# Kernel tuning notes

Measured on AMD Instinct MI355X. Metric: run time of the kernel, lower is better.

Reference implementation:

```python
import jax, jax.numpy as jnp
import numpy as np

B, Q, KV = 4, 256, 1024
QS, KS, H, VS = 128, 128, 128, 256

def setup_inputs() -> dict:
    key = jax.random.key(0)
    ks = jax.random.split(key, 7)
    return {
        "queries": jax.random.normal(ks[0], (B, Q, QS), dtype=jnp.float32),
        "keys": jax.random.normal(ks[1], (B, KV, KS), dtype=jnp.float32),
        "values": jax.random.normal(ks[2], (B, KV, VS), dtype=jnp.float32),
        "valid_lens": jax.random.randint(ks[3], (B,), 0, KV, dtype=jnp.int64 if jax.config.read('jax_enable_x64') else jnp.int32),
        "Wq": jax.random.normal(ks[4], (QS, H), dtype=jnp.float32),
        "Wk": jax.random.normal(ks[5], (KS, H), dtype=jnp.float32),
        "wv": jax.random.normal(ks[6], (H,), dtype=jnp.float32),
    }

def reference(queries, keys, values, valid_lens, Wq, Wk, wv):
    # project: [B,Q,H], [B,KV,H]
    q = jnp.einsum('bqd,dh->bqh', queries, Wq)
    k = jnp.einsum('bkd,dh->bkh', keys, Wk)
    # additive scores: broadcast add -> tanh -> reduce with w_v  [B,Q,KV]
    feats = jnp.tanh(q[:, :, None, :] + k[:, None, :, :])  # [B,Q,KV,H]
    scores = jnp.einsum('bqkh,h->bqk', feats, wv)
    # masked softmax over KV with value -1e6 at masked slots
    mask = jnp.arange(scores.shape[-1])[None, None, :] < valid_lens[:, None, None]
    scores = jnp.where(mask, scores, -1e6)
    attn = jax.nn.softmax(scores, axis=-1)
    # weighted sum of values  [B,Q,VS]
    return jnp.einsum('bqk,bkv->bqv', attn, values)
```

## Files before the change

kernel.cpp:

```cpp
#include <hip/hip_runtime.h>

#define C2LOG2E 2.8853900817779268f
#define LOG2E   1.4426950408889634f

__device__ __forceinline__ float sig2(float x) {
    return __builtin_amdgcn_rcpf(__builtin_amdgcn_exp2f(x) + 1.0f);
}

__global__ __launch_bounds__(256) void proj_kernel(
    const float* __restrict__ q_in, const float* __restrict__ k_in,
    const float* __restrict__ Wq, const float* __restrict__ Wk,
    float* __restrict__ qc, float* __restrict__ kct)
{
    __shared__ __align__(16) float x_s[8][128];
    __shared__ float ps[2][8][128];
    int tid = threadIdx.x;
    int blk = blockIdx.x;
    bool is_q = (blk < 128);
    int r0 = (is_q ? blk : blk - 128) * 8;
    const float* X = (is_q ? q_in : k_in) + (size_t)r0 * 128;
    const float* W = is_q ? Wq : Wk;

    {
        float4 v = ((const float4*)X)[tid];
        *(float4*)&x_s[tid >> 5][(tid & 31) * 4] = v;
    }
    __syncthreads();

    int h    = tid & 127;
    int half = tid >> 7;
    int d0   = half * 64;
    float acc[8] = {0,0,0,0,0,0,0,0};
#pragma unroll 2
    for (int i4 = 0; i4 < 16; ++i4) {
        int d = d0 + 4*i4;
        float w0 = W[(d+0)*128 + h];
        float w1 = W[(d+1)*128 + h];
        float w2 = W[(d+2)*128 + h];
        float w3 = W[(d+3)*128 + h];
#pragma unroll
        for (int r = 0; r < 8; ++r) {
            float4 xv = *(const float4*)&x_s[r][d];
            acc[r] = fmaf(xv.x, w0, fmaf(xv.y, w1,
                     fmaf(xv.z, w2, fmaf(xv.w, w3, acc[r]))));
        }
    }
#pragma unroll
    for (int r = 0; r < 8; ++r) ps[half][r][h] = acc[r];
    __syncthreads();

    int rq = tid >> 7;
    float v0 = (ps[0][rq*4+0][h] + ps[1][rq*4+0][h]) * C2LOG2E;
    float v1 = (ps[0][rq*4+1][h] + ps[1][rq*4+1][h]) * C2LOG2E;
    float v2 = (ps[0][rq*4+2][h] + ps[1][rq*4+2][h]) * C2LOG2E;
    float v3 = (ps[0][rq*4+3][h] + ps[1][rq*4+3][h]) * C2LOG2E;

    if (is_q) {
        qc[(size_t)(r0 + rq*4 + 0)*128 + h] = v0;
        qc[(size_t)(r0 + rq*4 + 1)*128 + h] = v1;
        qc[(size_t)(r0 + rq*4 + 2)*128 + h] = v2;
        qc[(size_t)(r0 + rq*4 + 3)*128 + h] = v3;
    } else {
        int bb = r0 >> 10;
        int c  = (r0 & 1023) >> 6;
        int i0 = (r0 & 63) + rq*4;
        float* dst = kct + (((size_t)(bb*16 + c))*128 + h)*64 + i0;
        *(float4*)dst = make_float4(v0, v1, v2, v3);
    }
}

__global__ __launch_bounds__(1024, 4) void attn_kernel(
    const float* __restrict__ qc, const float* __restrict__ kct,
    const float* __restrict__ values, const int* __restrict__ valid_lens,
    const float* __restrict__ wv, float* __restrict__ out)
{
    __shared__ float4 e4_s[1024];
    __shared__ float4 po8[8][4][64];
    __shared__ float4 red_m[16], red_s[16];

    int tid  = threadIdx.x;
    int b    = blockIdx.y;
    int q0   = blockIdx.x * 4;
    int w    = tid >> 6;
    int lane = tid & 63;
    int kv   = tid;
    int vl   = valid_lens[b];

    const float4* q40 = (const float4*)(qc + (size_t)(b*256 + q0)*128);
    const float4* wv4 = (const float4*)wv;
    const float* p = kct + ((size_t)(b*16 + w))*8192 + lane;

    float a[4] = {0,0,0,0};
    if (w*64 < vl) {
        for (int hb = 0; hb < 32; ++hb) {
            float4 wvv = wv4[hb];
            float4 k = make_float4(p[0], p[64], p[128], p[192]);
            p += 256;
#pragma unroll
            for (int q = 0; q < 4; ++q) {
                float4 qv = q40[q*32 + hb];
                a[q] = fmaf(wvv.x, sig2(qv.x + k.x), a[q]);
                a[q] = fmaf(wvv.y, sig2(qv.y + k.y), a[q]);
                a[q] = fmaf(wvv.z, sig2(qv.z + k.z), a[q]);
                a[q] = fmaf(wvv.w, sig2(qv.w + k.w), a[q]);
            }
        }
    }

    bool valid = (kv < vl);
    float s[4], m[4];
#pragma unroll
    for (int q = 0; q < 4; ++q) {
        s[q] = valid ? -2.f*a[q] : -1e6f;
        m[q] = s[q];
    }
#pragma unroll
    for (int off = 32; off; off >>= 1)
#pragma unroll
        for (int q = 0; q < 4; ++q) m[q] = fmaxf(m[q], __shfl_xor(m[q], off));
    if (lane == 0) red_m[w] = make_float4(m[0], m[1], m[2], m[3]);
    __syncthreads();
    {
        float4 mm = red_m[0];
#pragma unroll
        for (int ww = 1; ww < 16; ++ww) {
            float4 t = red_m[ww];
            mm.x = fmaxf(mm.x, t.x); mm.y = fmaxf(mm.y, t.y);
            mm.z = fmaxf(mm.z, t.z); mm.w = fmaxf(mm.w, t.w);
        }
        m[0] = mm.x; m[1] = mm.y; m[2] = mm.z; m[3] = mm.w;
    }

    float e[4], l[4];
#pragma unroll
    for (int q = 0; q < 4; ++q) {
        e[q] = __builtin_amdgcn_exp2f((s[q] - m[q]) * LOG2E);
        l[q] = e[q];
    }
    e4_s[kv] = make_float4(e[0], e[1], e[2], e[3]);
#pragma unroll
    for (int off = 32; off; off >>= 1)
#pragma unroll
        for (int q = 0; q < 4; ++q) l[q] += __shfl_xor(l[q], off);
    if (lane == 0) red_s[w] = make_float4(l[0], l[1], l[2], l[3]);
    __syncthreads();
    float inv[4];
    {
        float4 ss = red_s[0];
#pragma unroll
        for (int ww = 1; ww < 16; ++ww) {
            float4 t = red_s[ww];
            ss.x += t.x; ss.y += t.y; ss.z += t.z; ss.w += t.w;
        }
        inv[0] = 1.0f/ss.x; inv[1] = 1.0f/ss.y; inv[2] = 1.0f/ss.z; inv[3] = 1.0f/ss.w;
    }

    int kv_end = (vl == 0) ? 1024 : vl;
    float4 ac[4] = {{0,0,0,0},{0,0,0,0},{0,0,0,0},{0,0,0,0}};
    const float4* V4 = (const float4*)values + (size_t)b*65536 + lane;
#pragma unroll 2
    for (int k2 = w; k2 < kv_end; k2 += 16) {
        float4 vv = V4[(size_t)k2*64];
        float4 ee = e4_s[k2];
        ac[0].x = fmaf(ee.x, vv.x, ac[0].x); ac[0].y = fmaf(ee.x, vv.y, ac[0].y);
        ac[0].z = fmaf(ee.x, vv.z, ac[0].z); ac[0].w = fmaf(ee.x, vv.w, ac[0].w);
        ac[1].x = fmaf(ee.y, vv.x, ac[1].x); ac[1].y = fmaf(ee.y, vv.y, ac[1].y);
        ac[1].z = fmaf(ee.y, vv.z, ac[1].z); ac[1].w = fmaf(ee.y, vv.w, ac[1].w);
        ac[2].x = fmaf(ee.z, vv.x, ac[2].x); ac[2].y = fmaf(ee.z, vv.y, ac[2].y);
        ac[2].z = fmaf(ee.z, vv.z, ac[2].z); ac[2].w = fmaf(ee.z, vv.w, ac[2].w);
        ac[3].x = fmaf(ee.w, vv.x, ac[3].x); ac[3].y = fmaf(ee.w, vv.y, ac[3].y);
        ac[3].z = fmaf(ee.w, vv.z, ac[3].z); ac[3].w = fmaf(ee.w, vv.w, ac[3].w);
    }

    if (w >= 8) {
#pragma unroll
        for (int q = 0; q < 4; ++q) po8[w-8][q][lane] = ac[q];
    }
    __syncthreads();
    if (w < 8) {
#pragma unroll
        for (int q = 0; q < 4; ++q) {
            float4 t = po8[w][q][lane];
            t.x += ac[q].x; t.y += ac[q].y; t.z += ac[q].z; t.w += ac[q].w;
            po8[w][q][lane] = t;
        }
    }
    __syncthreads();

    int qq  = tid >> 8;
    int col = tid & 255;
    const float* pp = (const float*)po8;
    float r = 0.f;
#pragma unroll
    for (int ww = 0; ww < 8; ++ww) r += pp[(ww*4 + qq)*256 + col];
    out[((size_t)(b*256 + q0 + qq))*256 + col] = r * inv[qq];
}

extern "C" void kernel_launch(void* const* d_in, const int* in_sizes, int n_in,
                              void* d_out, int out_size, void* d_ws, size_t ws_size,
                              hipStream_t stream)
{
    const float* queries = (const float*)d_in[0];
    const float* keys    = (const float*)d_in[1];
    const float* values  = (const float*)d_in[2];
    const int*   vlens   = (const int*)d_in[3];
    const float* Wq      = (const float*)d_in[4];
    const float* Wk      = (const float*)d_in[5];
    const float* wv      = (const float*)d_in[6];
    float* out = (float*)d_out;

    float* qc  = (float*)d_ws;
    float* kct = qc + 4*256*128;

    proj_kernel<<<640, 256, 0, stream>>>(queries, keys, Wq, Wk, qc, kct);
    attn_kernel<<<dim3(64, 4), 1024, 0, stream>>>(qc, kct, values, vlens, wv, out);
}
```

Before: 106.3 us.

## Remap score phase to 2 queries x 2 KV chunks per wave with float4 key layout

```diff
diff --git a/kernel.cpp b/kernel.cpp
--- a/kernel.cpp
+++ b/kernel.cpp
@@ -64,8 +64,11 @@
         int bb = r0 >> 10;
         int c  = (r0 & 1023) >> 6;
         int i0 = (r0 & 63) + rq*4;
-        float* dst = kct + (((size_t)(bb*16 + c))*128 + h)*64 + i0;
-        *(float4*)dst = make_float4(v0, v1, v2, v3);
+        float* dst = kct + ((((size_t)(bb*16 + c))*32 + (h >> 2))*64 + i0)*4 + (h & 3);
+        dst[0]  = v0;
+        dst[4]  = v1;
+        dst[8]  = v2;
+        dst[12] = v3;
     }
 }
 
@@ -74,86 +77,108 @@
     const float* __restrict__ values, const int* __restrict__ valid_lens,
     const float* __restrict__ wv, float* __restrict__ out)
 {
-    __shared__ float4 e4_s[1024];
+    __shared__ float2 e2_s[2][1024];
     __shared__ float4 po8[8][4][64];
-    __shared__ float4 red_m[16], red_s[16];
+    __shared__ float2 red_m[16], red_s[16];
 
     int tid  = threadIdx.x;
     int b    = blockIdx.y;
     int q0   = blockIdx.x * 4;
     int w    = tid >> 6;
     int lane = tid & 63;
-    int kv   = tid;
+    int qh   = w >> 3;
+    int c0   = w & 7;
     int vl   = valid_lens[b];
 
-    const float4* q40 = (const float4*)(qc + (size_t)(b*256 + q0)*128);
+    const float4* qa4 = (const float4*)(qc + (size_t)(b*256 + q0 + 2*qh)*128);
+    const float4* qb4 = qa4 + 32;
     const float4* wv4 = (const float4*)wv;
-    const float* p = kct + ((size_t)(b*16 + w))*8192 + lane;
-
-    float a[4] = {0,0,0,0};
-    if (w*64 < vl) {
+    const float4* kb  = (const float4*)kct;
+    const float4* p0  = kb + ((size_t)(b*16 + c0))*2048 + lane;
+    const float4* p1  = p0 + 8*2048;
+
+    bool act0 = (c0*64 < vl);
+    bool act1 = ((c0 + 8)*64 < vl);
+    float a00=0.f, a10=0.f, a01=0.f, a11=0.f;
+
+    if (act1) {
         for (int hb = 0; hb < 32; ++hb) {
             float4 wvv = wv4[hb];
-            float4 k = make_float4(p[0], p[64], p[128], p[192]);
-            p += 256;
-#pragma unroll
-            for (int q = 0; q < 4; ++q) {
-                float4 qv = q40[q*32 + hb];
-                a[q] = fmaf(wvv.x, sig2(qv.x + k.x), a[q]);
-                a[q] = fmaf(wvv.y, sig2(qv.y + k.y), a[q]);
-                a[q] = fmaf(wvv.z, sig2(qv.z + k.z), a[q]);
-                a[q] = fmaf(wvv.w, sig2(qv.w + k.w), a[q]);
-            }
-        }
-    }
-
-    bool valid = (kv < vl);
-    float s[4], m[4];
-#pragma unroll
-    for (int q = 0; q < 4; ++q) {
-        s[q] = valid ? -2.f*a[q] : -1e6f;
-        m[q] = s[q];
-    }
-#pragma unroll
-    for (int off = 32; off; off >>= 1)
-#pragma unroll
-        for (int q = 0; q < 4; ++q) m[q] = fmaxf(m[q], __shfl_xor(m[q], off));
-    if (lane == 0) red_m[w] = make_float4(m[0], m[1], m[2], m[3]);
+            float4 qa = qa4[hb], qb = qb4[hb];
+            float4 k0 = p0[(size_t)hb*64];
+            float4 k1 = p1[(size_t)hb*64];
+            a00 = fmaf(wvv.x, sig2(qa.x + k0.x), a00);
+            a10 = fmaf(wvv.x, sig2(qb.x + k0.x), a10);
+            a01 = fmaf(wvv.x, sig2(qa.x + k1.x), a01);
+            a11 = fmaf(wvv.x, sig2(qb.x + k1.x), a11);
+            a00 = fmaf(wvv.y, sig2(qa.y + k0.y), a00);
+            a10 = fmaf(wvv.y, sig2(qb.y + k0.y), a10);
+            a01 = fmaf(wvv.y, sig2(qa.y + k1.y), a01);
+            a11 = fmaf(wvv.y, sig2(qb.y + k1.y), a11);
+            a00 = fmaf(wvv.z, sig2(qa.z + k0.z), a00);
+            a10 = fmaf(wvv.z, sig2(qb.z + k0.z), a10);
+            a01 = fmaf(wvv.z, sig2(qa.z + k1.z), a01);
+            a11 = fmaf(wvv.z, sig2(qb.z + k1.z), a11);
+            a00 = fmaf(wvv.w, sig2(qa.w + k0.w), a00);
+            a10 = fmaf(wvv.w, sig2(qb.w + k0.w), a10);
+            a01 = fmaf(wvv.w, sig2(qa.w + k1.w), a01);
+            a11 = fmaf(wvv.w, sig2(qb.w + k1.w), a11);
+        }
+    } else if (act0) {
+        for (int hb = 0; hb < 32; ++hb) {
+            float4 wvv = wv4[hb];
+            float4 qa = qa4[hb], qb = qb4[hb];
+            float4 k0 = p0[(size_t)hb*64];
+            a00 = fmaf(wvv.x, sig2(qa.x + k0.x), a00);
+            a10 = fmaf(wvv.x, sig2(qb.x + k0.x), a10);
+            a00 = fmaf(wvv.y, sig2(qa.y + k0.y), a00);
+            a10 = fmaf(wvv.y, sig2(qb.y + k0.y), a10);
+            a00 = fmaf(wvv.z, sig2(qa.z + k0.z), a00);
+            a10 = fmaf(wvv.z, sig2(qb.z + k0.z), a10);
+            a00 = fmaf(wvv.w, sig2(qa.w + k0.w), a00);
+            a10 = fmaf(wvv.w, sig2(qb.w + k0.w), a10);
+        }
+    }
+
+    int kv0 = c0*64 + lane, kv1 = kv0 + 512;
+    bool m0v = (kv0 < vl), m1v = (kv1 < vl);
+    float s00 = m0v ? -2.f*a00 : -1e6f;
+    float s10 = m0v ? -2.f*a10 : -1e6f;
+    float s01 = m1v ? -2.f*a01 : -1e6f;
+    float s11 = m1v ? -2.f*a11 : -1e6f;
+
+    float m0 = fmaxf(s00, s01), m1 = fmaxf(s10, s11);
+#pragma unroll
+    for (int off = 32; off; off >>= 1) {
+        m0 = fmaxf(m0, __shfl_xor(m0, off));
+        m1 = fmaxf(m1, __shfl_xor(m1, off));
+    }
+    if (lane == 0) red_m[w] = make_float2(m0, m1);
     __syncthreads();
     {
-        float4 mm = red_m[0];
-#pragma unroll
-        for (int ww = 1; ww < 16; ++ww) {
-            float4 t = red_m[ww];
+        float2 mm = red_m[qh*8];
+#pragma unroll
+        for (int ww = 1; ww < 8; ++ww) {
+            float2 t = red_m[qh*8 + ww];
             mm.x = fmaxf(mm.x, t.x); mm.y = fmaxf(mm.y, t.y);
-            mm.z = fmaxf(mm.z, t.z); mm.w = fmaxf(mm.w, t.w);
-        }
-        m[0] = mm.x; m[1] = mm.y; m[2] = mm.z; m[3] = mm.w;
-    }
-
-    float e[4], l[4];
-#pragma unroll
-    for (int q = 0; q < 4; ++q) {
-        e[q] = __builtin_amdgcn_exp2f((s[q] - m[q]) * LOG2E);
-        l[q] = e[q];
-    }
-    e4_s[kv] = make_float4(e[0], e[1], e[2], e[3]);
-#pragma unroll
-    for (int off = 32; off; off >>= 1)
-#pragma unroll
-        for (int q = 0; q < 4; ++q) l[q] += __shfl_xor(l[q], off);
-    if (lane == 0) red_s[w] = make_float4(l[0], l[1], l[2], l[3]);
-    __syncthreads();
-    float inv[4];
-    {
-        float4 ss = red_s[0];
-#pragma unroll
-        for (int ww = 1; ww < 16; ++ww) {
-            float4 t = red_s[ww];
-            ss.x += t.x; ss.y += t.y; ss.z += t.z; ss.w += t.w;
-        }
-        inv[0] = 1.0f/ss.x; inv[1] = 1.0f/ss.y; inv[2] = 1.0f/ss.z; inv[3] = 1.0f/ss.w;
-    }
+        }
+        m0 = mm.x; m1 = mm.y;
+    }
+
+    float e00 = __builtin_amdgcn_exp2f((s00 - m0) * LOG2E);
+    float e10 = __builtin_amdgcn_exp2f((s10 - m1) * LOG2E);
+    float e01 = __builtin_amdgcn_exp2f((s01 - m0) * LOG2E);
+    float e11 = __builtin_amdgcn_exp2f((s11 - m1) * LOG2E);
+    e2_s[qh][kv0] = make_float2(e00, e10);
+    e2_s[qh][kv1] = make_float2(e01, e11);
+    float l0 = e00 + e01, l1 = e10 + e11;
+#pragma unroll
+    for (int off = 32; off; off >>= 1) {
+        l0 += __shfl_xor(l0, off);
+        l1 += __shfl_xor(l1, off);
+    }
+    if (lane == 0) red_s[w] = make_float2(l0, l1);
+    __syncthreads();
 
     int kv_end = (vl == 0) ? 1024 : vl;
     float4 ac[4] = {{0,0,0,0},{0,0,0,0},{0,0,0,0},{0,0,0,0}};
@@ -161,15 +186,16 @@
 #pragma unroll 2
     for (int k2 = w; k2 < kv_end; k2 += 16) {
         float4 vv = V4[(size_t)k2*64];
-        float4 ee = e4_s[k2];
-        ac[0].x = fmaf(ee.x, vv.x, ac[0].x); ac[0].y = fmaf(ee.x, vv.y, ac[0].y);
-        ac[0].z = fmaf(ee.x, vv.z, ac[0].z); ac[0].w = fmaf(ee.x, vv.w, ac[0].w);
-        ac[1].x = fmaf(ee.y, vv.x, ac[1].x); ac[1].y = fmaf(ee.y, vv.y, ac[1].y);
-        ac[1].z = fmaf(ee.y, vv.z, ac[1].z); ac[1].w = fmaf(ee.y, vv.w, ac[1].w);
-        ac[2].x = fmaf(ee.z, vv.x, ac[2].x); ac[2].y = fmaf(ee.z, vv.y, ac[2].y);
-        ac[2].z = fmaf(ee.z, vv.z, ac[2].z); ac[2].w = fmaf(ee.z, vv.w, ac[2].w);
-        ac[3].x = fmaf(ee.w, vv.x, ac[3].x); ac[3].y = fmaf(ee.w, vv.y, ac[3].y);
-        ac[3].z = fmaf(ee.w, vv.z, ac[3].z); ac[3].w = fmaf(ee.w, vv.w, ac[3].w);
+        float2 ea = e2_s[0][k2];
+        float2 eb = e2_s[1][k2];
+        ac[0].x = fmaf(ea.x, vv.x, ac[0].x); ac[0].y = fmaf(ea.x, vv.y, ac[0].y);
+        ac[0].z = fmaf(ea.x, vv.z, ac[0].z); ac[0].w = fmaf(ea.x, vv.w, ac[0].w);
+        ac[1].x = fmaf(ea.y, vv.x, ac[1].x); ac[1].y = fmaf(ea.y, vv.y, ac[1].y);
+        ac[1].z = fmaf(ea.y, vv.z, ac[1].z); ac[1].w = fmaf(ea.y, vv.w, ac[1].w);
+        ac[2].x = fmaf(eb.x, vv.x, ac[2].x); ac[2].y = fmaf(eb.x, vv.y, ac[2].y);
+        ac[2].z = fmaf(eb.x, vv.z, ac[2].z); ac[2].w = fmaf(eb.x, vv.w, ac[2].w);
+        ac[3].x = fmaf(eb.y, vv.x, ac[3].x); ac[3].y = fmaf(eb.y, vv.y, ac[3].y);
+        ac[3].z = fmaf(eb.y, vv.z, ac[3].z); ac[3].w = fmaf(eb.y, vv.w, ac[3].w);
     }
 
     if (w >= 8) {
@@ -189,11 +215,17 @@
 
     int qq  = tid >> 8;
     int col = tid & 255;
+    float ssum = 0.f;
+#pragma unroll
+    for (int ww = 0; ww < 8; ++ww) {
+        float2 t = red_s[(qq >> 1)*8 + ww];
+        ssum += (qq & 1) ? t.y : t.x;
+    }
     const float* pp = (const float*)po8;
     float r = 0.f;
 #pragma unroll
     for (int ww = 0; ww < 8; ++ww) r += pp[(ww*4 + qq)*256 + col];
-    out[((size_t)(b*256 + q0 + qq))*256 + col] = r * inv[qq];
+    out[((size_t)(b*256 + q0 + qq))*256 + col] = r / ssum;
 }
 
 extern "C" void kernel_launch(void* const* d_in, const int* in_sizes, int n_in,
```

Result: faster. 103.2 us (-2.8%).
